# Optimization experiments

Hardware: AMD Instinct MI355X
Metric: run time of the kernel (lower is better)

Reference implementation:

```python
import jax, jax.numpy as jnp
import numpy as np

NUM_HOPS = 3

def _position_encoding(sentence_size, embedding_size):
    # Vectorized version of the double loop in the source.
    i = np.arange(1, embedding_size + 1, dtype=np.float32)[:, None]  # [E,1]
    j = np.arange(1, sentence_size + 1, dtype=np.float32)[None, :]   # [1,S]
    enc = (i - embedding_size / 2.0) * (j - sentence_size / 2.0)
    enc = 1.0 + 4.0 * enc / embedding_size / sentence_size
    return jnp.asarray(np.transpose(enc))  # [S, E]

def setup_inputs() -> dict:
    key = jax.random.key(0)
    ks = jax.random.split(key, 9)
    B, M, S, E, V, OUT = 16, 512, 32, 128, 32000, 128
    scale = 0.02
    return {
        "queries": jax.random.randint(ks[0], (B, S), 0, V, dtype=jnp.int32),
        "stories": jax.random.randint(ks[1], (B, M, S), 0, V, dtype=jnp.int32),
        "query_biases": jax.random.normal(ks[2], (V - 1, E), jnp.float32) * scale,
        "stories_biases": jax.random.normal(ks[3], (V - 1, E), jnp.float32) * scale,
        "memory_biases": jax.random.normal(ks[4], (M, E), jnp.float32) * scale,
        "output_biases": jax.random.normal(ks[5], (V - 1, E), jnp.float32) * scale,
        "w_intermediate": jax.random.normal(ks[6], (E, E), jnp.float32) * scale,
        "w_output": jax.random.normal(ks[7], (E, OUT), jnp.float32) * scale,
        "w_final": jax.random.normal(ks[8], (OUT, V), jnp.float32) * scale,
    }

def reference(queries, stories, query_biases, stories_biases, memory_biases,
              output_biases, w_intermediate, w_output, w_final):
    B, M, S = stories.shape
    E = query_biases.shape[1]
    enc = _position_encoding(S, E)  # [S, E]
    nil = jnp.zeros((1, E), dtype=query_biases.dtype)

    # Story memory: gather -> positional weight -> reduce over sentence axis.
    st_tab = jnp.concatenate([stories_biases, nil], axis=0)          # [V, E]
    mem_emb = st_tab[stories]                                        # [B,M,S,E]
    memory = jnp.einsum('bmse,se->bme', mem_emb, enc) + memory_biases

    # Query embedding.
    q_tab = jnp.concatenate([query_biases, nil], axis=0)
    q = jnp.einsum('bse,se->be', q_tab[queries], enc)                # [B,E]

    # Output memory.
    o_tab = jnp.concatenate([output_biases, nil], axis=0)
    output = jnp.einsum('bmse,se->bme', o_tab[stories], enc)         # [B,M,E]

    out_layer = q
    for hop in range(NUM_HOPS):
        probs = jax.nn.softmax(jnp.einsum('bme,be->bm', memory, q))  # [B,M]
        layer_out = jnp.einsum('bme,bm->be', output, probs)          # [B,E]
        w = w_output if hop == NUM_HOPS - 1 else w_intermediate
        out_layer = (q + layer_out) @ w
        q = out_layer                     # pre-nonlinearity state, as in source
        out_layer = jax.nn.relu(out_layer)

    return out_layer @ w_final            # [B, vocab]
```

## Files before the change

### kernel.cpp

```cpp
#include <hip/hip_runtime.h>

constexpr int kB  = 16;
constexpr int kM  = 512;
constexpr int kS  = 32;
constexpr int kE  = 128;
constexpr int kV  = 32000;
constexpr int kVN = kV - 1;

__global__ __launch_bounds__(256) void embed_stories_kernel(
    const int*   __restrict__ stories,
    const float* __restrict__ st_bias,
    const float* __restrict__ out_bias,
    const float* __restrict__ mem_bias,
    float*       __restrict__ memory,
    float*       __restrict__ output)
{
    __shared__ int sidx[2][kS];
    const int t     = threadIdx.x;
    const int pair0 = blockIdx.x * 2;
    if (t < 64) {
        const int p = t >> 5, s = t & 31;
        sidx[p][s] = stories[(pair0 + p) * kS + s];
    }
    __syncthreads();
    const int p  = t >> 7;
    const int e  = t & 127;
    const int bm = pair0 + p;
    const int m  = bm & (kM - 1);

    float accm = mem_bias[m * kE + e];
    float acco = 0.0f;
    const float ef = (float)(e - 63);
    #pragma unroll
    for (int s = 0; s < kS; ++s) {
        const int idx   = sidx[p][s];
        const float enc = 1.0f + ef * (float)(s - 15) * (1.0f / 1024.0f);
        if (idx < kVN) {
            const size_t off = (size_t)idx * kE + e;
            accm = fmaf(st_bias[off],  enc, accm);
            acco = fmaf(out_bias[off], enc, acco);
        }
    }
    memory[(size_t)bm * kE + e] = accm;
    output[(size_t)bm * kE + e] = acco;
}

__global__ __launch_bounds__(512) void hops_kernel(
    const int*   __restrict__ queries,
    const float* __restrict__ q_bias,
    const float* __restrict__ memory,
    const float* __restrict__ output,
    const float* __restrict__ w_int,
    const float* __restrict__ w_out,
    float*       __restrict__ x)
{
    __shared__ __align__(16) float q_s[kE];
    __shared__ float xbuf[kE];
    __shared__ float sc[kM];
    __shared__ float part[4][kE];
    __shared__ float red[8];
    __shared__ int   qidx[kS];

    const int b = blockIdx.x;
    const int t = threadIdx.x;

    if (t < kS) qidx[t] = queries[b * kS + t];
    __syncthreads();

    if (t < kE) {
        float acc = 0.0f;
        const float ef = (float)(t - 63);
        #pragma unroll
        for (int s = 0; s < kS; ++s) {
            const int idx   = qidx[s];
            const float enc = 1.0f + ef * (float)(s - 15) * (1.0f / 1024.0f);
            if (idx < kVN) acc = fmaf(q_bias[(size_t)idx * kE + t], enc, acc);
        }
        q_s[t] = acc;
    }
    __syncthreads();

    const float* memb = memory + (size_t)b * kM * kE;
    const float* outb = output + (size_t)b * kM * kE;
    const int g = t >> 7;
    const int e = t & 127;

    for (int hop = 0; hop < 3; ++hop) {
        const float4* row = (const float4*)(memb + (size_t)t * kE);
        const float4* qv  = (const float4*)q_s;
        float sv = 0.0f;
        #pragma unroll
        for (int i = 0; i < kE / 4; ++i) {
            const float4 a = row[i], q4 = qv[i];
            sv += a.x * q4.x + a.y * q4.y + a.z * q4.z + a.w * q4.w;
        }
        float v = sv;
        #pragma unroll
        for (int off = 32; off; off >>= 1) v = fmaxf(v, __shfl_down(v, off, 64));
        if ((t & 63) == 0) red[t >> 6] = v;
        __syncthreads();
        float mx = red[0];
        #pragma unroll
        for (int i = 1; i < 8; ++i) mx = fmaxf(mx, red[i]);
        const float ex = __expf(sv - mx);
        float sum = ex;
        #pragma unroll
        for (int off = 32; off; off >>= 1) sum += __shfl_down(sum, off, 64);
        __syncthreads();
        if ((t & 63) == 0) red[t >> 6] = sum;
        sc[t] = ex;
        __syncthreads();
        const float tot = red[0] + red[1] + red[2] + red[3] +
                          red[4] + red[5] + red[6] + red[7];
        const float inv = 1.0f / tot;

        float acc = 0.0f;
        const float* ob = outb + (size_t)g * 128 * kE;
        for (int mm = 0; mm < 128; ++mm)
            acc = fmaf(sc[g * 128 + mm], ob[(size_t)mm * kE + e], acc);
        part[g][e] = acc;
        __syncthreads();
        if (t < kE) {
            const float lo = (part[0][t] + part[1][t] + part[2][t] + part[3][t]) * inv;
            xbuf[t] = q_s[t] + lo;
        }
        __syncthreads();

        const float* w = (hop == 2) ? w_out : w_int;
        float acc2 = 0.0f;
        #pragma unroll 4
        for (int k = 0; k < 32; ++k) {
            const int ee = g * 32 + k;
            acc2 = fmaf(xbuf[ee], w[ee * kE + e], acc2);
        }
        part[g][e] = acc2;
        __syncthreads();
        if (t < kE) q_s[t] = part[0][t] + part[1][t] + part[2][t] + part[3][t];
        __syncthreads();
    }
    if (t < kE) x[b * kE + t] = fmaxf(q_s[t], 0.0f);
}

__global__ __launch_bounds__(256) void final_mm_kernel(
    const float* __restrict__ x,
    const float* __restrict__ wf,
    float*       __restrict__ out)
{
    __shared__ float xs[kB * kE];
    const int t = threadIdx.x;
    for (int i = t; i < kB * kE; i += 256) xs[i] = x[i];
    __syncthreads();

    const int v  = blockIdx.x * 256 + t;
    const int e0 = blockIdx.y * 32;
    float acc[kB];
    #pragma unroll
    for (int b = 0; b < kB; ++b) acc[b] = 0.0f;
    for (int e = e0; e < e0 + 32; ++e) {
        const float w = wf[(size_t)e * kV + v];
        #pragma unroll
        for (int b = 0; b < kB; ++b) acc[b] = fmaf(xs[b * kE + e], w, acc[b]);
    }
    #pragma unroll
    for (int b = 0; b < kB; ++b) atomicAdd(&out[(size_t)b * kV + v], acc[b]);
}

extern "C" void kernel_launch(void* const* d_in, const int* in_sizes, int n_in,
                              void* d_out, int out_size, void* d_ws, size_t ws_size,
                              hipStream_t stream)
{
    const int*   queries  = (const int*)  d_in[0];
    const int*   stories  = (const int*)  d_in[1];
    const float* q_bias   = (const float*)d_in[2];
    const float* st_bias  = (const float*)d_in[3];
    const float* mem_bias = (const float*)d_in[4];
    const float* out_bias = (const float*)d_in[5];
    const float* w_int    = (const float*)d_in[6];
    const float* w_out    = (const float*)d_in[7];
    const float* w_final  = (const float*)d_in[8];
    float* out = (float*)d_out;

    float* memory = (float*)d_ws;
    float* output = memory + (size_t)kB * kM * kE;
    float* x      = output + (size_t)kB * kM * kE;

    hipMemsetAsync(d_out, 0, (size_t)out_size * sizeof(float), stream);

    embed_stories_kernel<<<dim3((kB * kM) / 2), dim3(256), 0, stream>>>(
        stories, st_bias, out_bias, mem_bias, memory, output);

    hops_kernel<<<dim3(kB), dim3(512), 0, stream>>>(
        queries, q_bias, memory, output, w_int, w_out, x);

    final_mm_kernel<<<dim3(kV / 256, 4), dim3(256), 0, stream>>>(x, w_final, out);
}
```

Measured before the change: 186.2 us.

## Split hop loop across four cooperative blocks per batch with LDS-cached memory

Rewrites all three kernels. The embedding kernel now has each block cover 16 rows, one table and a 16-wide slice of the embedding dimension, with four independent accumulators per thread. The hop kernel now spreads each batch across four 1024-thread blocks launched cooperatively, caches each block's memory/output quarter in LDS, and syncs the blocks through global-atomic group barriers for the softmax and weighted-sum reductions. The final matmul drops the memset and atomics by reducing over the full embedding dimension per thread, reading a transposed activation buffer. This adds spin-wait barrier cost and a large LDS footprint per block in exchange for more parallelism in the serial hop stage.

New measurement: 324.2 us. 74.1% more time.

```diff
diff --git a/kernel.cpp b/kernel.cpp
--- a/kernel.cpp
+++ b/kernel.cpp
@@ -6,8 +6,9 @@
 constexpr int kE  = 128;
 constexpr int kV  = 32000;
 constexpr int kVN = kV - 1;
-
-__global__ __launch_bounds__(256) void embed_stories_kernel(
+constexpr int kMS = 132;
+
+__global__ __launch_bounds__(256) void embed_kernel(
     const int*   __restrict__ stories,
     const float* __restrict__ st_bias,
     const float* __restrict__ out_bias,
@@ -15,154 +16,238 @@
     float*       __restrict__ memory,
     float*       __restrict__ output)
 {
-    __shared__ int sidx[2][kS];
+    __shared__ int sidx[16 * kS];
     const int t     = threadIdx.x;
-    const int pair0 = blockIdx.x * 2;
-    if (t < 64) {
-        const int p = t >> 5, s = t & 31;
-        sidx[p][s] = stories[(pair0 + p) * kS + s];
-    }
-    __syncthreads();
-    const int p  = t >> 7;
-    const int e  = t & 127;
-    const int bm = pair0 + p;
-    const int m  = bm & (kM - 1);
-
-    float accm = mem_bias[m * kE + e];
-    float acco = 0.0f;
-    const float ef = (float)(e - 63);
-    #pragma unroll
-    for (int s = 0; s < kS; ++s) {
-        const int idx   = sidx[p][s];
-        const float enc = 1.0f + ef * (float)(s - 15) * (1.0f / 1024.0f);
-        if (idx < kVN) {
-            const size_t off = (size_t)idx * kE + e;
-            accm = fmaf(st_bias[off],  enc, accm);
-            acco = fmaf(out_bias[off], enc, acco);
-        }
-    }
-    memory[(size_t)bm * kE + e] = accm;
-    output[(size_t)bm * kE + e] = acco;
-}
-
-__global__ __launch_bounds__(512) void hops_kernel(
+    const int bid   = blockIdx.x;
+    const int combo = bid & 15;
+    const int rg    = bid >> 4;
+    const int tb    = combo >> 3;
+    const int ch    = combo & 7;
+
+    const int row0 = rg * 16;
+    sidx[t]       = stories[row0 * kS + t];
+    sidx[t + 256] = stories[row0 * kS + 256 + t];
+    __syncthreads();
+
+    const int r   = t >> 4;
+    const int l   = t & 15;
+    const int e   = ch * 16 + l;
+    const int row = row0 + r;
+    const float ef = (float)(e - 63) * (1.0f / 1024.0f);
+    const float* tab = tb ? out_bias : st_bias;
+    const int* si = sidx + r * kS;
+
+    float a0 = 0.f, a1 = 0.f, a2 = 0.f, a3 = 0.f;
+    #pragma unroll
+    for (int s = 0; s < kS; s += 4) {
+        const int i0 = si[s], i1 = si[s + 1], i2 = si[s + 2], i3 = si[s + 3];
+        if (i0 < kVN) a0 = fmaf(tab[(size_t)i0 * kE + e], fmaf(ef, (float)(s     - 15), 1.f), a0);
+        if (i1 < kVN) a1 = fmaf(tab[(size_t)i1 * kE + e], fmaf(ef, (float)(s + 1 - 15), 1.f), a1);
+        if (i2 < kVN) a2 = fmaf(tab[(size_t)i2 * kE + e], fmaf(ef, (float)(s + 2 - 15), 1.f), a2);
+        if (i3 < kVN) a3 = fmaf(tab[(size_t)i3 * kE + e], fmaf(ef, (float)(s + 3 - 15), 1.f), a3);
+    }
+    float acc = (a0 + a1) + (a2 + a3);
+    if (tb == 0) {
+        acc += mem_bias[(row & (kM - 1)) * kE + e];
+        memory[(size_t)row * kE + e] = acc;
+    } else {
+        output[(size_t)row * kE + e] = acc;
+    }
+}
+
+__device__ __forceinline__ void group_barrier(unsigned* ctr, unsigned target)
+{
+    __syncthreads();
+    if (threadIdx.x == 0) {
+        __threadfence();
+        __hip_atomic_fetch_add(ctr, 1u, __ATOMIC_ACQ_REL, __HIP_MEMORY_SCOPE_AGENT);
+        while (__hip_atomic_load(ctr, __ATOMIC_ACQUIRE, __HIP_MEMORY_SCOPE_AGENT) < target)
+            __builtin_amdgcn_s_sleep(8);
+    }
+    __syncthreads();
+    __threadfence();
+}
+
+__global__ __launch_bounds__(1024) void hops_kernel(
     const int*   __restrict__ queries,
     const float* __restrict__ q_bias,
     const float* __restrict__ memory,
     const float* __restrict__ output,
     const float* __restrict__ w_int,
     const float* __restrict__ w_out,
-    float*       __restrict__ x)
-{
+    float*       __restrict__ scores_g,
+    float*       __restrict__ lo_part,
+    float*       __restrict__ xg_t,
+    unsigned*    __restrict__ bar)
+{
+    __shared__ __align__(16) float mem_lds[128 * kMS];
+    __shared__ __align__(16) float out_lds[128 * kE];
+    __shared__ float sc_all[kM];
     __shared__ __align__(16) float q_s[kE];
-    __shared__ float xbuf[kE];
-    __shared__ float sc[kM];
-    __shared__ float part[4][kE];
-    __shared__ float red[8];
-    __shared__ int   qidx[kS];
-
-    const int b = blockIdx.x;
-    const int t = threadIdx.x;
-
+    __shared__ float xb[kE];
+    __shared__ __align__(16) float part8[8][kE];
+    __shared__ float red[16];
+    __shared__ int qidx[kS];
+
+    const int bid = blockIdx.x;
+    const int b   = bid >> 2;
+    const int qtr = bid & 3;
+    const int t   = threadIdx.x;
+    unsigned* ctr = bar + b;
+
+    const float* memb = memory + ((size_t)b * kM + qtr * 128) * kE;
+    const float* outb = output + ((size_t)b * kM + qtr * 128) * kE;
+    #pragma unroll
+    for (int i = 0; i < 4; ++i) {
+        const int flat = t + i * 1024;
+        const int rr = flat >> 5, ff = (flat & 31) * 4;
+        *(float4*)&mem_lds[rr * kMS + ff] = *(const float4*)&memb[(size_t)rr * kE + ff];
+        *(float4*)&out_lds[rr * kE  + ff] = *(const float4*)&outb[(size_t)rr * kE + ff];
+    }
     if (t < kS) qidx[t] = queries[b * kS + t];
     __syncthreads();
 
+    if (t < 256) {
+        const int g = t >> 5, lane = t & 31, e0 = lane * 4;
+        const float f0 = (float)(e0 - 63) * (1.0f / 1024.0f);
+        const float f1 = (float)(e0 - 62) * (1.0f / 1024.0f);
+        const float f2 = (float)(e0 - 61) * (1.0f / 1024.0f);
+        const float f3 = (float)(e0 - 60) * (1.0f / 1024.0f);
+        float4 a = {0.f, 0.f, 0.f, 0.f};
+        #pragma unroll
+        for (int j = 0; j < 4; ++j) {
+            const int s   = g * 4 + j;
+            const int idx = qidx[s];
+            const float sf = (float)(s - 15);
+            if (idx < kVN) {
+                const float4 v = *(const float4*)&q_bias[(size_t)idx * kE + e0];
+                a.x = fmaf(v.x, fmaf(f0, sf, 1.f), a.x);
+                a.y = fmaf(v.y, fmaf(f1, sf, 1.f), a.y);
+                a.z = fmaf(v.z, fmaf(f2, sf, 1.f), a.z);
+                a.w = fmaf(v.w, fmaf(f3, sf, 1.f), a.w);
+            }
+        }
+        *(float4*)&part8[g][e0] = a;
+    }
+    __syncthreads();
     if (t < kE) {
-        float acc = 0.0f;
-        const float ef = (float)(t - 63);
-        #pragma unroll
-        for (int s = 0; s < kS; ++s) {
-            const int idx   = qidx[s];
-            const float enc = 1.0f + ef * (float)(s - 15) * (1.0f / 1024.0f);
-            if (idx < kVN) acc = fmaf(q_bias[(size_t)idx * kE + t], enc, acc);
-        }
-        q_s[t] = acc;
-    }
-    __syncthreads();
-
-    const float* memb = memory + (size_t)b * kM * kE;
-    const float* outb = output + (size_t)b * kM * kE;
-    const int g = t >> 7;
-    const int e = t & 127;
-
+        float s = 0.f;
+        #pragma unroll
+        for (int g = 0; g < 8; ++g) s += part8[g][t];
+        q_s[t] = s;
+    }
+    __syncthreads();
+
+    unsigned barno = 0;
     for (int hop = 0; hop < 3; ++hop) {
-        const float4* row = (const float4*)(memb + (size_t)t * kE);
-        const float4* qv  = (const float4*)q_s;
-        float sv = 0.0f;
-        #pragma unroll
-        for (int i = 0; i < kE / 4; ++i) {
-            const float4 a = row[i], q4 = qv[i];
-            sv += a.x * q4.x + a.y * q4.y + a.z * q4.z + a.w * q4.w;
-        }
-        float v = sv;
-        #pragma unroll
-        for (int off = 32; off; off >>= 1) v = fmaxf(v, __shfl_down(v, off, 64));
-        if ((t & 63) == 0) red[t >> 6] = v;
+        {
+            const int rw = t >> 3, sub = t & 7;
+            const float4* qv = (const float4*)&q_s[sub * 16];
+            const float4* mv = (const float4*)&mem_lds[rw * kMS + sub * 16];
+            float d = 0.f;
+            #pragma unroll
+            for (int i = 0; i < 4; ++i) {
+                const float4 m4 = mv[i], q4 = qv[i];
+                d = fmaf(m4.x, q4.x, d); d = fmaf(m4.y, q4.y, d);
+                d = fmaf(m4.z, q4.z, d); d = fmaf(m4.w, q4.w, d);
+            }
+            d += __shfl_down(d, 4);
+            d += __shfl_down(d, 2);
+            d += __shfl_down(d, 1);
+            if (sub == 0) scores_g[b * kM + qtr * 128 + rw] = d;
+        }
+        group_barrier(ctr, 4 * (++barno));
+
+        const int wv_id = t >> 6, ln = t & 63;
+        const float sv = (t < kM) ? scores_g[b * kM + t] : -1e30f;
+        float mr = sv;
+        #pragma unroll
+        for (int off = 32; off; off >>= 1) mr = fmaxf(mr, __shfl_down(mr, off));
+        if (ln == 0) red[wv_id] = mr;
         __syncthreads();
         float mx = red[0];
         #pragma unroll
         for (int i = 1; i < 8; ++i) mx = fmaxf(mx, red[i]);
-        const float ex = __expf(sv - mx);
-        float sum = ex;
-        #pragma unroll
-        for (int off = 32; off; off >>= 1) sum += __shfl_down(sum, off, 64);
-        __syncthreads();
-        if ((t & 63) == 0) red[t >> 6] = sum;
-        sc[t] = ex;
-        __syncthreads();
-        const float tot = red[0] + red[1] + red[2] + red[3] +
-                          red[4] + red[5] + red[6] + red[7];
+        const float ex = (t < kM) ? __expf(sv - mx) : 0.f;
+        float sr = ex;
+        #pragma unroll
+        for (int off = 32; off; off >>= 1) sr += __shfl_down(sr, off);
+        __syncthreads();
+        if (ln == 0) red[wv_id] = sr;
+        __syncthreads();
+        float tot = 0.f;
+        #pragma unroll
+        for (int i = 0; i < 8; ++i) tot += red[i];
         const float inv = 1.0f / tot;
-
-        float acc = 0.0f;
-        const float* ob = outb + (size_t)g * 128 * kE;
-        for (int mm = 0; mm < 128; ++mm)
-            acc = fmaf(sc[g * 128 + mm], ob[(size_t)mm * kE + e], acc);
-        part[g][e] = acc;
+        if (t < kM) sc_all[t] = ex * inv;
+        __syncthreads();
+
+        {
+            const int e = t & 127, grp = t >> 7;
+            const float* pp = &sc_all[qtr * 128 + grp * 16];
+            const float* ob = &out_lds[grp * 16 * kE + e];
+            float acc = 0.f;
+            #pragma unroll
+            for (int j = 0; j < 16; ++j)
+                acc = fmaf(pp[j], ob[j * kE], acc);
+            part8[grp][e] = acc;
+        }
         __syncthreads();
         if (t < kE) {
-            const float lo = (part[0][t] + part[1][t] + part[2][t] + part[3][t]) * inv;
-            xbuf[t] = q_s[t] + lo;
-        }
-        __syncthreads();
-
-        const float* w = (hop == 2) ? w_out : w_int;
-        float acc2 = 0.0f;
-        #pragma unroll 4
-        for (int k = 0; k < 32; ++k) {
-            const int ee = g * 32 + k;
-            acc2 = fmaf(xbuf[ee], w[ee * kE + e], acc2);
-        }
-        part[g][e] = acc2;
-        __syncthreads();
-        if (t < kE) q_s[t] = part[0][t] + part[1][t] + part[2][t] + part[3][t];
-        __syncthreads();
-    }
-    if (t < kE) x[b * kE + t] = fmaxf(q_s[t], 0.0f);
-}
-
-__global__ __launch_bounds__(256) void final_mm_kernel(
-    const float* __restrict__ x,
+            float s = 0.f;
+            #pragma unroll
+            for (int g = 0; g < 8; ++g) s += part8[g][t];
+            lo_part[((size_t)b * 4 + qtr) * kE + t] = s;
+        }
+        group_barrier(ctr, 4 * (++barno));
+
+        if (t < kE) {
+            const float* lp = &lo_part[(size_t)b * 4 * kE];
+            xb[t] = q_s[t] + lp[t] + lp[kE + t] + lp[2 * kE + t] + lp[3 * kE + t];
+        }
+        __syncthreads();
+        {
+            const float* w = (hop == 2) ? w_out : w_int;
+            const int e = t & 127, grp = t >> 7;
+            float acc = 0.f;
+            #pragma unroll
+            for (int j = 0; j < 16; ++j) {
+                const int k = grp * 16 + j;
+                acc = fmaf(xb[k], w[k * kE + e], acc);
+            }
+            part8[grp][e] = acc;
+        }
+        __syncthreads();
+        if (t < kE) {
+            float s = 0.f;
+            #pragma unroll
+            for (int g = 0; g < 8; ++g) s += part8[g][t];
+            q_s[t] = s;
+        }
+        __syncthreads();
+    }
+
+    if (qtr == 0 && t < kE) xg_t[t * kB + b] = fmaxf(q_s[t], 0.f);
+}
+
+__global__ __launch_bounds__(256) void final_kernel(
+    const float* __restrict__ xg_t,
     const float* __restrict__ wf,
     float*       __restrict__ out)
 {
-    __shared__ float xs[kB * kE];
-    const int t = threadIdx.x;
-    for (int i = t; i < kB * kE; i += 256) xs[i] = x[i];
-    __syncthreads();
-
-    const int v  = blockIdx.x * 256 + t;
-    const int e0 = blockIdx.y * 32;
+    const int v = blockIdx.x * 256 + threadIdx.x;
     float acc[kB];
     #pragma unroll
-    for (int b = 0; b < kB; ++b) acc[b] = 0.0f;
-    for (int e = e0; e < e0 + 32; ++e) {
-        const float w = wf[(size_t)e * kV + v];
-        #pragma unroll
-        for (int b = 0; b < kB; ++b) acc[b] = fmaf(xs[b * kE + e], w, acc[b]);
-    }
-    #pragma unroll
-    for (int b = 0; b < kB; ++b) atomicAdd(&out[(size_t)b * kV + v], acc[b]);
+    for (int b = 0; b < kB; ++b) acc[b] = 0.f;
+    #pragma unroll 4
+    for (int e = 0; e < kE; ++e) {
+        const float wv = wf[(size_t)e * kV + v];
+        const float* xr = xg_t + e * kB;
+        #pragma unroll
+        for (int b = 0; b < kB; ++b) acc[b] = fmaf(xr[b], wv, acc[b]);
+    }
+    #pragma unroll
+    for (int b = 0; b < kB; ++b) out[(size_t)b * kV + v] = acc[b];
 }
 
 extern "C" void kernel_launch(void* const* d_in, const int* in_sizes, int n_in,
@@ -180,17 +265,25 @@
     const float* w_final  = (const float*)d_in[8];
     float* out = (float*)d_out;
 
-    float* memory = (float*)d_ws;
-    float* output = memory + (size_t)kB * kM * kE;
-    float* x      = output + (size_t)kB * kM * kE;
-
-    hipMemsetAsync(d_out, 0, (size_t)out_size * sizeof(float), stream);
-
-    embed_stories_kernel<<<dim3((kB * kM) / 2), dim3(256), 0, stream>>>(
+    float* memory   = (float*)d_ws;
+    float* output   = memory   + (size_t)kB * kM * kE;
+    float* scores_g = output   + (size_t)kB * kM * kE;
+    float* lo_part  = scores_g + (size_t)kB * kM;
+    float* xg_t     = lo_part  + (size_t)kB * 4 * kE;
+    unsigned* bar   = (unsigned*)(xg_t + (size_t)kE * kB);
+
+    hipMemsetAsync(bar, 0, kB * sizeof(unsigned), stream);
+
+    embed_kernel<<<dim3(8192), dim3(256), 0, stream>>>(
         stories, st_bias, out_bias, mem_bias, memory, output);
 
-    hops_kernel<<<dim3(kB), dim3(512), 0, stream>>>(
-        queries, q_bias, memory, output, w_int, w_out, x);
-
-    final_mm_kernel<<<dim3(kV / 256, 4), dim3(256), 0, stream>>>(x, w_final, out);
-}
+    void* args[] = {
+        (void*)&queries, (void*)&q_bias, (void*)&memory, (void*)&output,
+        (void*)&w_int, (void*)&w_out, (void*)&scores_g, (void*)&lo_part,
+        (void*)&xg_t, (void*)&bar
+    };
+    hipLaunchCooperativeKernel((const void*)hops_kernel,
+                               dim3(64), dim3(1024), args, 0, stream);
+
+    final_kernel<<<dim3(kV / 256), dim3(256), 0, stream>>>(xg_t, w_final, out);
+}
```
